# Optimization experiments

Measured on AMD Instinct MI355X. Metric: run time of the kernel, lower is better.

## Reference

```python
import jax, jax.numpy as jnp
import numpy as np

N_NODES = 50000
N_EDGES = 800000


def gcn_conv(x, edge_index, W, b, n_nodes):
    """PyG GCNConv: h = x @ W; add self-loops; symmetric D^-1/2 A D^-1/2 aggregation; + bias."""
    h = x @ W  # [N, out]
    loops = jnp.arange(n_nodes, dtype=edge_index.dtype)
    row = jnp.concatenate([edge_index[0], loops])  # source nodes
    col = jnp.concatenate([edge_index[1], loops])  # target nodes
    deg = jax.ops.segment_sum(jnp.ones_like(col, dtype=h.dtype), col, num_segments=n_nodes)
    deg_inv_sqrt = jnp.where(deg > 0, jax.lax.rsqrt(deg), 0.0)
    norm = deg_inv_sqrt[row] * deg_inv_sqrt[col]  # [E+N]
    msg = h[row] * norm[:, None]  # gather + scale
    out = jax.ops.segment_sum(msg, col, num_segments=n_nodes)  # scatter-add
    return out + b


def setup_inputs() -> dict:
    key = jax.random.key(0)
    k_x, k_ei, k_w1, k_w2 = jax.random.split(key, 4)
    x = jax.random.normal(k_x, (N_NODES, 9), dtype=jnp.float32)
    edge_index = jax.random.randint(k_ei, (2, N_EDGES), 0, N_NODES, dtype=jnp.int64)
    # Glorot-like init for the linear weights
    W1 = jax.random.normal(k_w1, (9, 100), dtype=jnp.float32) * (1.0 / np.sqrt(9.0))
    b1 = jnp.zeros((100,), dtype=jnp.float32)
    W2 = jax.random.normal(k_w2, (100, 1), dtype=jnp.float32) * (1.0 / np.sqrt(100.0))
    b2 = jnp.zeros((1,), dtype=jnp.float32)
    return {"x": x, "edge_index": edge_index, "W1": W1, "b1": b1, "W2": W2, "b2": b2}


def reference(x, edge_index, W1, b1, W2, b2):
    n = x.shape[0]
    h = jax.nn.relu(gcn_conv(x, edge_index, W1, b1, n))
    return gcn_conv(h, edge_index, W2, b2, n)  # [N, 1]
```

## Files before the change

### kernel.cpp

```cpp
#include <hip/hip_runtime.h>

#define N_NODES 50000
#define N_EDGES 800000
#define FIN 9
#define FH 100
#define XS_W 12
#define NP 256
#define NPB 196
#define EPB_A 2048
#define NCHUNK ((N_EDGES + EPB_A - 1) / EPB_A)
#define RCAP 28
#define PREG (NCHUNK * RCAP)
#define SCAP 3584
#define GL 8

template <int BS>
__device__ __forceinline__ int block_incl_scan(int val, int t, int* wsum) {
    int lane = t & 63;
#pragma unroll
    for (int off = 1; off < 64; off <<= 1) {
        int v2 = __shfl_up(val, off);
        if (lane >= off) val += v2;
    }
    if (lane == 63) wsum[t >> 6] = val;
    __syncthreads();
    int add = 0;
#pragma unroll
    for (int w = 0; w < BS / 64; ++w)
        if (w < (t >> 6)) add += wsum[w];
    val += add;
    __syncthreads();
    return val;
}

__global__ __launch_bounds__(512) void k_partA(const int* __restrict__ row,
                                               const int* __restrict__ col,
                                               int* __restrict__ ghist,
                                               int* __restrict__ part_ebuf, int e) {
    __shared__ int hist[NP];
    __shared__ int scn[NP];
    __shared__ int cur[NP];
    __shared__ int stage[EPB_A];
    __shared__ int wsum[8];
    int t = threadIdx.x;
    int chunk = blockIdx.x;
    int e0 = chunk * EPB_A;
    int nE = min(EPB_A, e - e0);
    if (t < NP) hist[t] = 0;
    __syncthreads();

    int epack[EPB_A / 512];
    int cntl = 0;
    for (int i = t; i < nE; i += 512) {
        int r = row[e0 + i], c = col[e0 + i];
        int p = c / NPB;
        int ln = c - p * NPB;
        epack[cntl++] = (r << 16) | (p << 8) | ln;
        atomicAdd(&hist[p], 1);
    }
    __syncthreads();
    int d = (t < NP) ? hist[t] : 0;
    int incl = block_incl_scan<512>(d, t, wsum);
    int excl = incl - d;
    if (t < NP) { scn[t] = excl; cur[t] = excl; }
    __syncthreads();
    for (int i = 0; i < cntl; ++i) {
        unsigned u = (unsigned)epack[i];
        int L = atomicAdd(&cur[(u >> 8) & 255], 1);
        stage[L] = (int)u;
    }
    __syncthreads();
    for (int s = t; s < nE; s += 512) {
        int u = stage[s];
        int p = ((unsigned)u >> 8) & 255;
        int idx = s - scn[p];
        if (idx < RCAP) part_ebuf[p * PREG + chunk * RCAP + idx] = u;
    }
    if (t < NP) ghist[t * NCHUNK + chunk] = min(hist[t], RCAP);
}

__global__ __launch_bounds__(512) void k_partB(const int* __restrict__ ghist,
                                               int* __restrict__ part_ebuf,
                                               const float* __restrict__ x,
                                               int* __restrict__ start,
                                               int* __restrict__ cnt,
                                               float* __restrict__ xs, int n) {
    __shared__ int cc[NCHUNK];
    __shared__ int hist[NP];
    __shared__ int scn[NP];
    __shared__ int cur[NP];
    __shared__ int stageR[SCAP];
    __shared__ int wsum[8];
    __shared__ int sm_tot;
    int t = threadIdx.x;
    int p = blockIdx.x;
    for (int i = t; i < NCHUNK; i += 512) cc[i] = ghist[p * NCHUNK + i];
    if (t < NP) hist[t] = 0;
    __syncthreads();

    int g  = t / GL;
    int lg = t % GL;
    for (int c = g; c < NCHUNK; c += 512 / GL) {
        int base = p * PREG + c * RCAP;
        int m = cc[c];
        for (int k = lg; k < m; k += GL) {
            unsigned u = (unsigned)part_ebuf[base + k];
            atomicAdd(&hist[u & 255], 1);
        }
    }
    __syncthreads();
    int d = (t < NP) ? hist[t] : 0;
    int incl = block_incl_scan<512>(d, t, wsum);
    int excl = incl - d;
    if (t < NP) { scn[t] = excl; cur[t] = excl; }
    if (t == NP - 1) sm_tot = incl;
    __syncthreads();
    for (int c = g; c < NCHUNK; c += 512 / GL) {
        int base = p * PREG + c * RCAP;
        int m = cc[c];
        for (int k = lg; k < m; k += GL) {
            unsigned u = (unsigned)part_ebuf[base + k];
            int L = atomicAdd(&cur[u & 255], 1);
            if (L < SCAP) stageR[L] = (int)(u >> 16);
        }
    }
    __syncthreads();
    int mt = min(sm_tot, SCAP);
    for (int s = t; s < mt; s += 512) part_ebuf[p * PREG + s] = stageR[s];

    int v = p * NPB + t;
    if (t < NPB && v < n) {
        int dd = hist[t];
        start[v] = p * PREG + scn[t];
        cnt[v] = dd;
        float dv = rsqrtf((float)(dd + 1));
        float* xr = &xs[(size_t)v * XS_W];
#pragma unroll
        for (int k = 0; k < FIN; ++k) xr[k] = dv * x[v * FIN + k];
        xr[9] = dv; xr[10] = 0.0f; xr[11] = 0.0f;
    }
}

__global__ __launch_bounds__(256) void k_gather16(const float4* __restrict__ xs4,
                                                  const int* __restrict__ csr,
                                                  const int* __restrict__ start,
                                                  const int* __restrict__ cnt,
                                                  const float* __restrict__ W1,
                                                  const float* __restrict__ b1,
                                                  const float* __restrict__ W2,
                                                  float* __restrict__ ps, int n) {
    __shared__ float sW1[FIN * FH];
    __shared__ float sb1[FH];
    __shared__ float sW2[FH];
    int t = threadIdx.x;
    for (int i = t; i < FIN * FH; i += 256) sW1[i] = W1[i];
    for (int i = t; i < FH; i += 256) { sb1[i] = b1[i]; sW2[i] = W2[i]; }
    __syncthreads();

    int idx = blockIdx.x * 256 + t;
    int v = idx >> 4;
    int l = t & 15;
    if (v >= n) return;

    float4 a0 = make_float4(0, 0, 0, 0), a1 = a0;
    float a8 = 0.0f;
    int s = start[v], m = cnt[v];
    for (int j = l; j < m; j += 16) {
        int r = csr[s + j];
        float4 q0 = xs4[r * 3], q1 = xs4[r * 3 + 1], q2 = xs4[r * 3 + 2];
        a0.x += q0.x; a0.y += q0.y; a0.z += q0.z; a0.w += q0.w;
        a1.x += q1.x; a1.y += q1.y; a1.z += q1.z; a1.w += q1.w;
        a8 += q2.x;
    }
#pragma unroll
    for (int off = 1; off < 16; off <<= 1) {
        a0.x += __shfl_xor(a0.x, off); a0.y += __shfl_xor(a0.y, off);
        a0.z += __shfl_xor(a0.z, off); a0.w += __shfl_xor(a0.w, off);
        a1.x += __shfl_xor(a1.x, off); a1.y += __shfl_xor(a1.y, off);
        a1.z += __shfl_xor(a1.z, off); a1.w += __shfl_xor(a1.w, off);
        a8   += __shfl_xor(a8, off);
    }
    float4 s0 = xs4[v * 3], s1 = xs4[v * 3 + 1], s2 = xs4[v * 3 + 2];
    float dv = s2.y;
    float xa[FIN];
    xa[0] = dv * (a0.x + s0.x); xa[1] = dv * (a0.y + s0.y);
    xa[2] = dv * (a0.z + s0.z); xa[3] = dv * (a0.w + s0.w);
    xa[4] = dv * (a1.x + s1.x); xa[5] = dv * (a1.y + s1.y);
    xa[6] = dv * (a1.z + s1.z); xa[7] = dv * (a1.w + s1.w);
    xa[8] = dv * (a8 + s2.x);

    float pv = 0.0f;
    for (int j = l; j < FH; j += 16) {
        float h = sb1[j];
#pragma unroll
        for (int k = 0; k < FIN; ++k) h = fmaf(xa[k], sW1[k * FH + j], h);
        h = fmaxf(h, 0.0f);
        pv = fmaf(h, sW2[j], pv);
    }
    pv += __shfl_xor(pv, 1);
    pv += __shfl_xor(pv, 2);
    pv += __shfl_xor(pv, 4);
    pv += __shfl_xor(pv, 8);
    if (l == 0) ps[v] = dv * pv;
}

__global__ __launch_bounds__(256) void k_out16(const int* __restrict__ csr,
                                               const int* __restrict__ start,
                                               const int* __restrict__ cnt,
                                               const float* __restrict__ ps,
                                               const float* __restrict__ xs,
                                               const float* __restrict__ b2,
                                               float* __restrict__ out, int n) {
    int t = threadIdx.x;
    int idx = blockIdx.x * 256 + t;
    int v = idx >> 4;
    int l = t & 15;
    if (v >= n) return;
    int s = start[v], m = cnt[v];
    float sum = 0.0f;
    for (int j = l; j < m; j += 16) sum += ps[csr[s + j]];
    sum += __shfl_xor(sum, 1);
    sum += __shfl_xor(sum, 2);
    sum += __shfl_xor(sum, 4);
    sum += __shfl_xor(sum, 8);
    if (l == 0) {
        float dv = xs[(size_t)v * XS_W + 9];
        out[v] = dv * (sum + ps[v]) + b2[0];
    }
}

__global__ void k_count(const int* __restrict__ col, int* __restrict__ ideg, int e) {
    int i = blockIdx.x * blockDim.x + threadIdx.x;
    if (i < e) atomicAdd(&ideg[col[i]], 1);
}
__global__ void k_offsets(const int* __restrict__ ideg, int* __restrict__ start,
                          int* __restrict__ cursor, float* __restrict__ dinv,
                          int* __restrict__ counter, int n) {
    __shared__ int sdata[256];
    __shared__ int sbase;
    int t = threadIdx.x;
    int v = blockIdx.x * 256 + t;
    int d = (v < n) ? ideg[v] : 0;
    sdata[t] = d;
    __syncthreads();
    for (int off = 1; off < 256; off <<= 1) {
        int tmp = (t >= off) ? sdata[t - off] : 0;
        __syncthreads();
        sdata[t] += tmp;
        __syncthreads();
    }
    if (t == 255) sbase = atomicAdd(counter, sdata[255]);
    __syncthreads();
    if (v < n) {
        int excl = sdata[t] - d;
        start[v] = sbase + excl;
        cursor[v] = sbase + excl;
        dinv[v] = rsqrtf((float)(d + 1));
    }
}
__global__ void k_bucket(const int* __restrict__ row, const int* __restrict__ col,
                         int* __restrict__ cursor, int* __restrict__ csr, int e) {
    int i = blockIdx.x * blockDim.x + threadIdx.x;
    if (i >= e) return;
    int pos = atomicAdd(&cursor[col[i]], 1);
    csr[pos] = row[i];
}
__global__ void k_gather_dense(const float* __restrict__ x, const int* __restrict__ csr,
                               const int* __restrict__ start, const int* __restrict__ ideg,
                               const float* __restrict__ dinv, const float* __restrict__ W1,
                               const float* __restrict__ b1, const float* __restrict__ W2,
                               float* __restrict__ p, int n) {
    __shared__ float sW1[FIN * FH];
    __shared__ float sb1[FH];
    __shared__ float sW2[FH];
    int t = threadIdx.x;
    for (int i = t; i < FIN * FH; i += blockDim.x) sW1[i] = W1[i];
    for (int i = t; i < FH; i += blockDim.x) { sb1[i] = b1[i]; sW2[i] = W2[i]; }
    __syncthreads();
    int v = blockIdx.x * blockDim.x + t;
    if (v >= n) return;
    float acc[FIN];
#pragma unroll
    for (int k = 0; k < FIN; ++k) acc[k] = 0.0f;
    int s = start[v], cntv = ideg[v];
    for (int j = 0; j < cntv; ++j) {
        int r = csr[s + j];
        float w = dinv[r];
#pragma unroll
        for (int k = 0; k < FIN; ++k) acc[k] = fmaf(w, x[r * FIN + k], acc[k]);
    }
    float dvv = dinv[v];
    float self = dvv * dvv;
    float xa[FIN];
#pragma unroll
    for (int k = 0; k < FIN; ++k) xa[k] = acc[k] * dvv + x[v * FIN + k] * self;
    float pv = 0.0f;
    for (int j = 0; j < FH; ++j) {
        float h = sb1[j];
#pragma unroll
        for (int k = 0; k < FIN; ++k) h = fmaf(xa[k], sW1[k * FH + j], h);
        h = fmaxf(h, 0.0f);
        pv = fmaf(h, sW2[j], pv);
    }
    p[v] = pv;
}
__global__ void k_out(const int* __restrict__ csr, const int* __restrict__ start,
                      const int* __restrict__ ideg, const float* __restrict__ dinv,
                      const float* __restrict__ p, const float* __restrict__ b2,
                      float* __restrict__ out, int n) {
    int v = blockIdx.x * blockDim.x + threadIdx.x;
    if (v >= n) return;
    int s = start[v], cntv = ideg[v];
    float sum = 0.0f;
    for (int j = 0; j < cntv; ++j) sum = fmaf(dinv[csr[s + j]], p[csr[s + j]], sum);
    float dvv = dinv[v];
    out[v] = dvv * sum + p[v] * dvv * dvv + b2[0];
}

extern "C" void kernel_launch(void* const* d_in, const int* in_sizes, int n_in,
                              void* d_out, int out_size, void* d_ws, size_t ws_size,
                              hipStream_t stream) {
    const float* x  = (const float*)d_in[0];
    const int*   ei = (const int*)d_in[1];
    const float* W1 = (const float*)d_in[2];
    const float* b1 = (const float*)d_in[3];
    const float* W2 = (const float*)d_in[4];
    const float* b2 = (const float*)d_in[5];
    float* out = (float*)d_out;

    const int n = N_NODES;
    const int e = N_EDGES;
    const int* row = ei;
    const int* col = ei + e;

    const int B = 256;
    int gn = (n + B - 1) / B;
    int gn16 = (16 * n + B - 1) / B;
    int ge = (e + B - 1) / B;

    size_t need = ((size_t)n * (XS_W + 3) + (size_t)NP * NCHUNK + (size_t)NP * PREG) * sizeof(int);
    if (ws_size >= need) {
        float* xs      = (float*)d_ws;
        int* startA    = (int*)(xs + (size_t)n * XS_W);
        int* cntA      = startA + n;
        float* ps      = (float*)(cntA + n);
        int* ghist     = (int*)(ps + n);
        int* part_ebuf = ghist + (size_t)NP * NCHUNK;

        k_partA<<<NCHUNK, 512, 0, stream>>>(row, col, ghist, part_ebuf, e);
        k_partB<<<NP, 512, 0, stream>>>(ghist, part_ebuf, x, startA, cntA, xs, n);
        k_gather16<<<gn16, B, 0, stream>>>((const float4*)xs, part_ebuf, startA, cntA,
                                           W1, b1, W2, ps, n);
        k_out16<<<gn16, B, 0, stream>>>(part_ebuf, startA, cntA, ps, xs, b2, out, n);
    } else {
        int* ideg    = (int*)d_ws;
        int* counter = ideg + n;
        int* startA  = counter + 1;
        int* cursor  = startA + n;
        float* dinv  = (float*)(cursor + n);
        float* p     = dinv + n;
        int* csr     = (int*)(p + n);

        hipMemsetAsync(ideg, 0, (size_t)(n + 1) * sizeof(int), stream);
        k_count<<<ge, B, 0, stream>>>(col, ideg, e);
        k_offsets<<<gn, B, 0, stream>>>(ideg, startA, cursor, dinv, counter, n);
        k_bucket<<<ge, B, 0, stream>>>(row, col, cursor, csr, e);
        k_gather_dense<<<gn, B, 0, stream>>>(x, csr, startA, ideg, dinv, W1, b1, W2, p, n);
        k_out<<<gn, B, 0, stream>>>(csr, startA, ideg, dinv, p, b2, out, n);
    }
}
```

Measured before the change: 47.65 us.

## Stage partition edges in LDS once and emit 16-bit CSR indices

The partition-B kernel now reads each partition's edge runs from global memory once into a compacted shared-memory buffer, using a scan over chunk counts. It then builds both the histogram and the scatter from that buffer, where it used to read global memory twice. The CSR source indices are stored as unsigned 16-bit values, which halves the index traffic for the gather and output kernels, and start offsets are now counted in 16-bit units. The gather kernel also moves to 1024-thread blocks. The 16-bit indices only hold because node ids stay below 65536, and the larger shared footprint and blocks may reduce occupancy.

```diff
diff --git a/kernel.cpp b/kernel.cpp
--- a/kernel.cpp
+++ b/kernel.cpp
@@ -86,52 +86,59 @@
                                                int* __restrict__ cnt,
                                                float* __restrict__ xs, int n) {
     __shared__ int cc[NCHUNK];
+    __shared__ int co[NCHUNK];
+    __shared__ int runsL[SCAP];
+    __shared__ unsigned short stage16[SCAP];
     __shared__ int hist[NP];
     __shared__ int scn[NP];
     __shared__ int cur[NP];
-    __shared__ int stageR[SCAP];
     __shared__ int wsum[8];
-    __shared__ int sm_tot;
     int t = threadIdx.x;
     int p = blockIdx.x;
     for (int i = t; i < NCHUNK; i += 512) cc[i] = ghist[p * NCHUNK + i];
     if (t < NP) hist[t] = 0;
     __syncthreads();
 
-    int g  = t / GL;
-    int lg = t % GL;
-    for (int c = g; c < NCHUNK; c += 512 / GL) {
-        int base = p * PREG + c * RCAP;
-        int m = cc[c];
-        for (int k = lg; k < m; k += GL) {
-            unsigned u = (unsigned)part_ebuf[base + k];
-            atomicAdd(&hist[u & 255], 1);
+    int c0 = (t < NCHUNK) ? cc[t] : 0;
+    int cincl = block_incl_scan<512>(c0, t, wsum);
+    if (t < NCHUNK) co[t] = cincl - c0;
+    __shared__ int sm_tot;
+    if (t == 511) sm_tot = cincl;
+    __syncthreads();
+    int tot = min(sm_tot, SCAP);
+
+    {
+        int g = t / GL, lg = t % GL;
+        for (int c = g; c < NCHUNK; c += 512 / GL) {
+            int base = p * PREG + c * RCAP;
+            int o = co[c], m = cc[c];
+            for (int k = lg; k < m; k += GL) {
+                int dst = o + k;
+                if (dst < SCAP) runsL[dst] = part_ebuf[base + k];
+            }
         }
     }
+    __syncthreads();
+    for (int i = t; i < tot; i += 512) atomicAdd(&hist[((unsigned)runsL[i]) & 255], 1);
     __syncthreads();
     int d = (t < NP) ? hist[t] : 0;
     int incl = block_incl_scan<512>(d, t, wsum);
     int excl = incl - d;
     if (t < NP) { scn[t] = excl; cur[t] = excl; }
-    if (t == NP - 1) sm_tot = incl;
-    __syncthreads();
-    for (int c = g; c < NCHUNK; c += 512 / GL) {
-        int base = p * PREG + c * RCAP;
-        int m = cc[c];
-        for (int k = lg; k < m; k += GL) {
-            unsigned u = (unsigned)part_ebuf[base + k];
-            int L = atomicAdd(&cur[u & 255], 1);
-            if (L < SCAP) stageR[L] = (int)(u >> 16);
-        }
-    }
-    __syncthreads();
-    int mt = min(sm_tot, SCAP);
-    for (int s = t; s < mt; s += 512) part_ebuf[p * PREG + s] = stageR[s];
+    __syncthreads();
+    for (int i = t; i < tot; i += 512) {
+        unsigned u = (unsigned)runsL[i];
+        int L = atomicAdd(&cur[u & 255], 1);
+        if (L < SCAP) stage16[L] = (unsigned short)(u >> 16);
+    }
+    __syncthreads();
+    unsigned short* csr16 = (unsigned short*)part_ebuf;
+    for (int s = t; s < tot; s += 512) csr16[(size_t)p * (2 * PREG) + s] = stage16[s];
 
     int v = p * NPB + t;
     if (t < NPB && v < n) {
         int dd = hist[t];
-        start[v] = p * PREG + scn[t];
+        start[v] = p * (2 * PREG) + scn[t];
         cnt[v] = dd;
         float dv = rsqrtf((float)(dd + 1));
         float* xr = &xs[(size_t)v * XS_W];
@@ -141,23 +148,23 @@
     }
 }
 
-__global__ __launch_bounds__(256) void k_gather16(const float4* __restrict__ xs4,
-                                                  const int* __restrict__ csr,
-                                                  const int* __restrict__ start,
-                                                  const int* __restrict__ cnt,
-                                                  const float* __restrict__ W1,
-                                                  const float* __restrict__ b1,
-                                                  const float* __restrict__ W2,
-                                                  float* __restrict__ ps, int n) {
+__global__ __launch_bounds__(1024) void k_gather16(const float4* __restrict__ xs4,
+                                                   const unsigned short* __restrict__ csr,
+                                                   const int* __restrict__ start,
+                                                   const int* __restrict__ cnt,
+                                                   const float* __restrict__ W1,
+                                                   const float* __restrict__ b1,
+                                                   const float* __restrict__ W2,
+                                                   float* __restrict__ ps, int n) {
     __shared__ float sW1[FIN * FH];
     __shared__ float sb1[FH];
     __shared__ float sW2[FH];
     int t = threadIdx.x;
-    for (int i = t; i < FIN * FH; i += 256) sW1[i] = W1[i];
-    for (int i = t; i < FH; i += 256) { sb1[i] = b1[i]; sW2[i] = W2[i]; }
-    __syncthreads();
-
-    int idx = blockIdx.x * 256 + t;
+    for (int i = t; i < FIN * FH; i += 1024) sW1[i] = W1[i];
+    if (t < FH) { sb1[t] = b1[t]; sW2[t] = W2[t]; }
+    __syncthreads();
+
+    int idx = blockIdx.x * 1024 + t;
     int v = idx >> 4;
     int l = t & 15;
     if (v >= n) return;
@@ -204,7 +211,7 @@
     if (l == 0) ps[v] = dv * pv;
 }
 
-__global__ __launch_bounds__(256) void k_out16(const int* __restrict__ csr,
+__global__ __launch_bounds__(256) void k_out16(const unsigned short* __restrict__ csr,
                                                const int* __restrict__ start,
                                                const int* __restrict__ cnt,
                                                const float* __restrict__ ps,
@@ -335,7 +342,8 @@
 
     const int B = 256;
     int gn = (n + B - 1) / B;
-    int gn16 = (16 * n + B - 1) / B;
+    int gn16a = (16 * n + 1023) / 1024;
+    int gn16b = (16 * n + B - 1) / B;
     int ge = (e + B - 1) / B;
 
     size_t need = ((size_t)n * (XS_W + 3) + (size_t)NP * NCHUNK + (size_t)NP * PREG) * sizeof(int);
@@ -349,9 +357,11 @@
 
         k_partA<<<NCHUNK, 512, 0, stream>>>(row, col, ghist, part_ebuf, e);
         k_partB<<<NP, 512, 0, stream>>>(ghist, part_ebuf, x, startA, cntA, xs, n);
-        k_gather16<<<gn16, B, 0, stream>>>((const float4*)xs, part_ebuf, startA, cntA,
-                                           W1, b1, W2, ps, n);
-        k_out16<<<gn16, B, 0, stream>>>(part_ebuf, startA, cntA, ps, xs, b2, out, n);
+        k_gather16<<<gn16a, 1024, 0, stream>>>((const float4*)xs,
+                                               (const unsigned short*)part_ebuf,
+                                               startA, cntA, W1, b1, W2, ps, n);
+        k_out16<<<gn16b, B, 0, stream>>>((const unsigned short*)part_ebuf,
+                                         startA, cntA, ps, xs, b2, out, n);
     } else {
         int* ideg    = (int*)d_ws;
         int* counter = ideg + n;
```

Measured after the change: 49.82 us. +4.6%, slower.
